# Kernel tuning notes

Hardware: AMD Instinct MI355X
Metric: run time of the kernel (lower is better)

## Reference

```python
import jax, jax.numpy as jnp
import numpy as np

B, N, D, H = 32, 512, 1024, 16
HD = D // H          # head_dim = 64
SEG = 64             # seg_num (router set size, softmax axis)
FACTOR = N           # einsum forces factor == seq_len


def setup_inputs() -> dict:
    key = jax.random.key(0)
    ks = jax.random.split(key, 12)
    s = 0.02
    return {
        "query": jax.random.normal(ks[0], (B, N, D), jnp.float32),
        "key":   jax.random.normal(ks[1], (B, N, D), jnp.float32),
        "value": jax.random.normal(ks[2], (B, N, D), jnp.float32),
        "router": jax.random.normal(ks[3], (SEG, FACTOR, HD), jnp.float32),
        "Wq": jax.random.normal(ks[4], (D, D), jnp.float32) * s,
        "bq": jnp.zeros((D,), jnp.float32),
        "Wk": jax.random.normal(ks[5], (D, D), jnp.float32) * s,
        "bk": jnp.zeros((D,), jnp.float32),
        "Wv": jax.random.normal(ks[6], (D, D), jnp.float32) * s,
        "bv": jnp.zeros((D,), jnp.float32),
        "Wo": jax.random.normal(ks[7], (D, D), jnp.float32) * s,
        "bo": jnp.zeros((D,), jnp.float32),
    }


def reference(query, key, value, router, Wq, bq, Wk, bk, Wv, bv, Wo, bo):
    b = query.shape[0]
    q = query @ Wq + bq                      # (B, N, D)
    k = key @ Wk + bk                        # computed but unused (faithful to source)
    v = value @ Wv + bv                      # computed but unused (faithful to source)
    # (B, N, H, HD) -> (B, H, N, HD)
    qh = q.reshape(b, -1, H, HD).transpose(0, 2, 1, 3)
    # torch: einsum('bnhd,bfhd->bnhf', q_bHnd, router_bSFd); shared 'h' = seq/factor
    # scores: (B, H, N, SEG); softmax over router/segment axis
    scores = jnp.einsum('bhnd,snd->bhns', qh, router)
    attn = jax.nn.softmax(scores, axis=-1)   # dropout = identity (eval mode)
    # combine: (B, H, N, HD)
    received = jnp.einsum('bhns,snd->bhnd', attn, router)
    received = received.transpose(0, 2, 1, 3).reshape(b, -1, D)
    output = received @ Wo + bo              # (B, N, D)
    return output, attn
```

## Files before the change

### kernel.cpp

```cpp
#include <hip/hip_runtime.h>

#define DEV __device__ __forceinline__

typedef __attribute__((ext_vector_type(8))) short bf16x8;
typedef __attribute__((ext_vector_type(4))) float f32x4;

constexpr int Bc  = 32;
constexpr int Nc  = 512;
constexpr int Dc  = 1024;
constexpr int Hc  = 16;
constexpr int HDc = 64;
constexpr int SEGc= 64;
constexpr int Mrows = Bc * Nc;

DEV unsigned short bf16r(float x) {
  union { float f; unsigned int u; } c; c.f = x;
  unsigned int r = (c.u + 0x7fffu + ((c.u >> 16) & 1u)) >> 16;
  return (unsigned short)r;
}

DEV void async_ld16(const void* g, void* l) {
  __builtin_amdgcn_global_load_lds(
      (const __attribute__((address_space(1))) void*)g,
      (__attribute__((address_space(3))) void*)l,
      16, 0, 0);
}

__global__ void cvt_bf16(const float* __restrict__ src,
                         unsigned short* __restrict__ dst, int n4) {
  int i = blockIdx.x * blockDim.x + threadIdx.x;
  if (i >= n4) return;
  float4 v = ((const float4*)src)[i];
  ushort4 o;
  o.x = bf16r(v.x); o.y = bf16r(v.y); o.z = bf16r(v.z); o.w = bf16r(v.w);
  ((ushort4*)dst)[i] = o;
}

__global__ void transpose_bf16(const float* __restrict__ src,
                               unsigned short* __restrict__ dst) {
  __shared__ float tile[32][33];
  int bx = blockIdx.x & 31, by = blockIdx.x >> 5;
  int tx = threadIdx.x & 31, ty = threadIdx.x >> 5;
  for (int i = 0; i < 4; ++i) {
    int r = ty + i * 8;
    tile[r][tx] = src[(size_t)(by * 32 + r) * 1024 + bx * 32 + tx];
  }
  __syncthreads();
  for (int i = 0; i < 4; ++i) {
    int r = ty + i * 8;
    dst[(size_t)(bx * 32 + r) * 1024 + by * 32 + tx] = bf16r(tile[tx][r]);
  }
}

template <bool OUT_F32>
__global__ __launch_bounds__(256)
void gemm_bt(const unsigned short* __restrict__ A,
             const unsigned short* __restrict__ BT,
             const float* __restrict__ bias,
             void* __restrict__ Cout) {
  constexpr int K = 1024, Nn = 1024, BM = 128, BN = 128, BK = 32;
  __shared__ unsigned short As[BM * BK];
  __shared__ unsigned short Bs[BN * BK];
  const int tid = threadIdx.x, lane = tid & 63, wave = tid >> 6;
  const int tm = blockIdx.x >> 3, tn = blockIdx.x & 7;
  const int wm = (wave >> 1) * 64, wn = (wave & 1) * 64;
  const int la = lane & 15, quad = lane >> 4, lb8 = quad * 8;

  f32x4 acc[4][4] = {};

  const int srow = tid >> 2;
  const int scol = (tid & 3) * 8;
  const unsigned short* Ag = A  + (size_t)(tm * BM + srow) * K + scol;
  const unsigned short* Bg = BT + (size_t)(tn * BN + srow) * K + scol;
  unsigned short* ldsA = As + wave * 512;
  unsigned short* ldsB = Bs + wave * 512;

  for (int k0 = 0; k0 < K; k0 += BK) {
    __syncthreads();
    async_ld16(Ag + k0,          ldsA);
    async_ld16(Ag + 64 * K + k0, ldsA + 2048);
    async_ld16(Bg + k0,          ldsB);
    async_ld16(Bg + 64 * K + k0, ldsB + 2048);
    __syncthreads();

    bf16x8 af[4], bfr[4];
#pragma unroll
    for (int i = 0; i < 4; ++i)
      af[i] = *(const bf16x8*)(As + (wm + i * 16 + la) * BK + lb8);
#pragma unroll
    for (int j = 0; j < 4; ++j)
      bfr[j] = *(const bf16x8*)(Bs + (wn + j * 16 + la) * BK + lb8);
#pragma unroll
    for (int i = 0; i < 4; ++i)
#pragma unroll
      for (int j = 0; j < 4; ++j)
        acc[i][j] = __builtin_amdgcn_mfma_f32_16x16x32_bf16(af[i], bfr[j],
                                                            acc[i][j], 0, 0, 0);
  }

  const int colbase = tn * BN + wn;
  float bv[4];
#pragma unroll
  for (int j = 0; j < 4; ++j) bv[j] = bias[colbase + j * 16 + la];

  float* eps = (wave < 2) ? ((float*)As) + wave * 1024
                          : ((float*)Bs) + (wave - 2) * 1024;
  const int rowbase = tm * BM + wm;

#pragma unroll
  for (int i = 0; i < 4; ++i) {
    __syncthreads();
#pragma unroll
    for (int j = 0; j < 4; ++j)
#pragma unroll
      for (int r = 0; r < 4; ++r)
        eps[(quad * 4 + r) * 64 + j * 16 + la] = acc[i][j][r] + bv[j];
    __syncthreads();
#pragma unroll
    for (int s = 0; s < 4; ++s) {
      int idx = s * 64 + lane;
      int row = idx >> 4, c4 = idx & 15;
      float4 v = *(const float4*)(eps + row * 64 + c4 * 4);
      size_t goff = (size_t)(rowbase + i * 16 + row) * Nn + colbase + c4 * 4;
      if (OUT_F32) {
        *(float4*)((float*)Cout + goff) = v;
      } else {
        ushort4 u;
        u.x = bf16r(v.x); u.y = bf16r(v.y); u.z = bf16r(v.z); u.w = bf16r(v.w);
        *(ushort4*)((unsigned short*)Cout + goff) = u;
      }
    }
  }
}

__global__ __launch_bounds__(256)
void router_mid(const unsigned short* __restrict__ qb,
                const unsigned short* __restrict__ routerb,
                float* __restrict__ attn_out,
                unsigned short* __restrict__ recv_out) {
  __shared__ unsigned short Rs [SEGc * HDc];
  __shared__ unsigned short RTs[HDc * SEGc];
  __shared__ unsigned short AT [4 * 16 * 64];
  __shared__ float          FW [4 * 16 * 64];

  const int n = blockIdx.x >> 1, half = blockIdx.x & 1;
  const int tid = threadIdx.x, lane = tid & 63, wave = tid >> 6;
  const int la = lane & 15, quad = lane >> 4, lb8 = quad * 8;

  {
    int c8 = (tid & 7) * 8;
    int s  = tid >> 3;
    async_ld16(routerb + ((size_t)s        * Nc + n) * HDc + c8, Rs + wave * 512);
    async_ld16(routerb + ((size_t)(s + 32) * Nc + n) * HDc + c8, Rs + 2048 + wave * 512);
  }
  __syncthreads();
  for (int i = 0; i < 16; ++i) {
    int idx = tid * 16 + i;
    RTs[(idx & 63) * 64 + (idx >> 6)] = Rs[idx];
  }
  __syncthreads();

  bf16x8 bs[4][2], br[4][2];
#pragma unroll
  for (int t = 0; t < 4; ++t)
#pragma unroll
    for (int kc = 0; kc < 2; ++kc) {
      bs[t][kc] = *(const bf16x8*)(Rs  + (t * 16 + la) * 64 + kc * 32 + lb8);
      br[t][kc] = *(const bf16x8*)(RTs + (t * 16 + la) * 64 + kc * 32 + lb8);
    }

  unsigned short* ATw = AT + wave * 1024;
  float*          FWw = FW + wave * 1024;

  for (int it = 0; it < 4; ++it) {
    const int bidx = half * 16 + wave * 4 + it;
    const unsigned short* qrow = qb + ((size_t)(bidx * Nc + n)) * Dc + la * 64;
    bf16x8 aq0 = *(const bf16x8*)(qrow + lb8);
    bf16x8 aq1 = *(const bf16x8*)(qrow + 32 + lb8);

    f32x4 sacc[4] = {};
#pragma unroll
    for (int t = 0; t < 4; ++t) {
      sacc[t] = __builtin_amdgcn_mfma_f32_16x16x32_bf16(aq0, bs[t][0], sacc[t], 0, 0, 0);
      sacc[t] = __builtin_amdgcn_mfma_f32_16x16x32_bf16(aq1, bs[t][1], sacc[t], 0, 0, 0);
    }

#pragma unroll
    for (int r = 0; r < 4; ++r) {
      float mx = fmaxf(fmaxf(sacc[0][r], sacc[1][r]), fmaxf(sacc[2][r], sacc[3][r]));
#pragma unroll
      for (int off = 1; off < 16; off <<= 1) mx = fmaxf(mx, __shfl_xor(mx, off));
      float e0 = __expf(sacc[0][r] - mx), e1 = __expf(sacc[1][r] - mx);
      float e2 = __expf(sacc[2][r] - mx), e3 = __expf(sacc[3][r] - mx);
      float sum = e0 + e1 + e2 + e3;
#pragma unroll
      for (int off = 1; off < 16; off <<= 1) sum += __shfl_xor(sum, off);
      float inv = 1.0f / sum;
      e0 *= inv; e1 *= inv; e2 *= inv; e3 *= inv;

      const int hrow = quad * 4 + r;
      float* fw = FWw + hrow * 64 + la;
      fw[0] = e0; fw[16] = e1; fw[32] = e2; fw[48] = e3;
      unsigned short* aw = ATw + hrow * 64 + la;
      aw[0] = bf16r(e0); aw[16] = bf16r(e1); aw[32] = bf16r(e2); aw[48] = bf16r(e3);
    }

    __asm__ volatile("s_waitcnt lgkmcnt(0)" ::: "memory");
    bf16x8 ar0 = *(const bf16x8*)(ATw + la * 64 + lb8);
    bf16x8 ar1 = *(const bf16x8*)(ATw + la * 64 + 32 + lb8);

    f32x4 racc[4] = {};
#pragma unroll
    for (int t = 0; t < 4; ++t) {
      racc[t] = __builtin_amdgcn_mfma_f32_16x16x32_bf16(ar0, br[t][0], racc[t], 0, 0, 0);
      racc[t] = __builtin_amdgcn_mfma_f32_16x16x32_bf16(ar1, br[t][1], racc[t], 0, 0, 0);
    }

#pragma unroll
    for (int s = 0; s < 4; ++s) {
      int idx = s * 64 + lane;
      int row = idx >> 4, c4 = idx & 15;
      float4 v = *(const float4*)(FWw + row * 64 + c4 * 4);
      *(float4*)(attn_out + ((size_t)(bidx * 16 + row) * Nc + n) * SEGc + c4 * 4) = v;
    }

#pragma unroll
    for (int r = 0; r < 4; ++r) {
      const int h = quad * 4 + r;
      unsigned short* aw = ATw + h * 64 + la;
#pragma unroll
      for (int t = 0; t < 4; ++t) aw[t * 16] = bf16r(racc[t][r]);
    }
    __asm__ volatile("s_waitcnt lgkmcnt(0)" ::: "memory");
    unsigned short* ro = recv_out + ((size_t)(bidx * Nc + n)) * Dc;
#pragma unroll
    for (int s = 0; s < 2; ++s)
      *(bf16x8*)(ro + s * 512 + lane * 8) = *(const bf16x8*)(ATw + s * 512 + lane * 8);
  }
}

extern "C" void kernel_launch(void* const* d_in, const int* in_sizes, int n_in,
                              void* d_out, int out_size, void* d_ws, size_t ws_size,
                              hipStream_t stream) {
  const float* query  = (const float*)d_in[0];
  const float* router = (const float*)d_in[3];
  const float* Wq     = (const float*)d_in[4];
  const float* bq     = (const float*)d_in[5];
  const float* Wo     = (const float*)d_in[10];
  const float* bo     = (const float*)d_in[11];

  float* out      = (float*)d_out;
  float* attn_out = out + (size_t)Bc * Nc * Dc;

  char* ws = (char*)d_ws;
  unsigned short* query_b  = (unsigned short*)(ws);
  unsigned short* q_b      = (unsigned short*)(ws + 33554432);
  unsigned short* recv_b   = (unsigned short*)(ws + 2u * 33554432);
  unsigned short* router_b = (unsigned short*)(ws + 3u * 33554432);
  unsigned short* WqT      = (unsigned short*)(ws + 3u * 33554432 + 4194304);
  unsigned short* WoT      = (unsigned short*)(ws + 3u * 33554432 + 4194304 + 2097152);

  cvt_bf16<<<16384, 256, 0, stream>>>(query,  query_b,  (Mrows * Dc) / 4);
  cvt_bf16<<<2048,  256, 0, stream>>>(router, router_b, (SEGc * Nc * HDc) / 4);
  transpose_bf16<<<1024, 256, 0, stream>>>(Wq, WqT);
  transpose_bf16<<<1024, 256, 0, stream>>>(Wo, WoT);

  gemm_bt<false><<<(Mrows / 128) * 8, 256, 0, stream>>>(query_b, WqT, bq, q_b);
  router_mid<<<2 * Nc, 256, 0, stream>>>(q_b, router_b, attn_out, recv_b);
  gemm_bt<true ><<<(Mrows / 128) * 8, 256, 0, stream>>>(recv_b, WoT, bo, out);
}
```

Before: 400.4 us.

## Fuse Q projection with router softmax mixing and pre-tile router weights

Replaces the separate query bf16 conversion, Q GEMM and router_mid kernels with one fused kernel. Each block computes the full 1024-wide Q projection for two sequence positions across all batches, converting query fp32 to bf16 on the fly with double-buffered LDS. It then runs the router score, softmax and combine steps straight from registers. This removes the round trips for the bf16 query copy and the q intermediate, but only 256 blocks of 512 threads are launched, which may underfill the GPU. It also uses a large LDS footprint and heavy accumulator register pressure.

```diff
diff --git a/kernel.cpp b/kernel.cpp
--- a/kernel.cpp
+++ b/kernel.cpp
@@ -24,16 +24,6 @@
       (const __attribute__((address_space(1))) void*)g,
       (__attribute__((address_space(3))) void*)l,
       16, 0, 0);
-}
-
-__global__ void cvt_bf16(const float* __restrict__ src,
-                         unsigned short* __restrict__ dst, int n4) {
-  int i = blockIdx.x * blockDim.x + threadIdx.x;
-  if (i >= n4) return;
-  float4 v = ((const float4*)src)[i];
-  ushort4 o;
-  o.x = bf16r(v.x); o.y = bf16r(v.y); o.z = bf16r(v.z); o.w = bf16r(v.w);
-  ((ushort4*)dst)[i] = o;
 }
 
 __global__ void transpose_bf16(const float* __restrict__ src,
@@ -52,15 +42,74 @@
   }
 }
 
+__global__ void wq_tile(const float* __restrict__ src,
+                        unsigned short* __restrict__ dst) {
+  __shared__ float tile[32][33];
+  int bx = blockIdx.x & 31, by = blockIdx.x >> 5;
+  int tx = threadIdx.x & 31, ty = threadIdx.x >> 5;
+  for (int i = 0; i < 4; ++i) {
+    int r = ty + i * 8;
+    tile[r][tx] = src[(size_t)(by * 32 + r) * 1024 + bx * 32 + tx];
+  }
+  __syncthreads();
+  if (ty < 4) {
+    int oct = ty;
+    unsigned short tmp[8];
+#pragma unroll
+    for (int e = 0; e < 8; ++e) tmp[e] = bf16r(tile[oct * 8 + e][tx]);
+    ushort4 u0, u1;
+    u0.x = tmp[0]; u0.y = tmp[1]; u0.z = tmp[2]; u0.w = tmp[3];
+    u1.x = tmp[4]; u1.y = tmp[5]; u1.z = tmp[6]; u1.w = tmp[7];
+    size_t idx = (size_t)by * 32768 + (size_t)oct * 8192 + (size_t)(bx * 32 + tx) * 8;
+    *(ushort4*)(dst + idx) = u0;
+    *(ushort4*)(dst + idx + 4) = u1;
+  }
+}
+
+__global__ void cvt_router2(const float* __restrict__ src,
+                            unsigned short* __restrict__ Rg,
+                            unsigned short* __restrict__ RTg) {
+  int nn = blockIdx.x;
+  int t  = threadIdx.x;
+  int s  = t >> 2, dq = (t & 3) * 16;
+  const float* p = src + ((size_t)s * 512 + nn) * 64 + dq;
+  float v[16];
+#pragma unroll
+  for (int i = 0; i < 16; i += 4) {
+    float4 f = *(const float4*)(p + i);
+    v[i] = f.x; v[i+1] = f.y; v[i+2] = f.z; v[i+3] = f.w;
+  }
+  unsigned short bv[16];
+#pragma unroll
+  for (int i = 0; i < 16; ++i) bv[i] = bf16r(v[i]);
+  unsigned short* rb = Rg + (size_t)nn * 4096 + s * 64;
+#pragma unroll
+  for (int o2 = 0; o2 < 2; ++o2) {
+    int oct  = (dq >> 3) + o2;
+    int phys = oct ^ (s & 7);
+    ushort4 a, b2;
+    a.x  = bv[o2*8+0]; a.y  = bv[o2*8+1]; a.z  = bv[o2*8+2]; a.w  = bv[o2*8+3];
+    b2.x = bv[o2*8+4]; b2.y = bv[o2*8+5]; b2.z = bv[o2*8+6]; b2.w = bv[o2*8+7];
+    *(ushort4*)(rb + phys * 8)     = a;
+    *(ushort4*)(rb + phys * 8 + 4) = b2;
+  }
+  unsigned short* tb = RTg + (size_t)nn * 4096;
+#pragma unroll
+  for (int i = 0; i < 16; ++i) {
+    int d = dq + i;
+    tb[d * 64 + (((s >> 3) ^ (d & 7)) * 8) + (s & 7)] = bv[i];
+  }
+}
+
 template <bool OUT_F32>
 __global__ __launch_bounds__(256)
 void gemm_bt(const unsigned short* __restrict__ A,
              const unsigned short* __restrict__ BT,
              const float* __restrict__ bias,
              void* __restrict__ Cout) {
-  constexpr int K = 1024, Nn = 1024, BM = 128, BN = 128, BK = 32;
+  constexpr int K = 1024, Nn = 1024, BM = 128, BK = 32;
   __shared__ unsigned short As[BM * BK];
-  __shared__ unsigned short Bs[BN * BK];
+  __shared__ unsigned short Bs[BM * BK];
   const int tid = threadIdx.x, lane = tid & 63, wave = tid >> 6;
   const int tm = blockIdx.x >> 3, tn = blockIdx.x & 7;
   const int wm = (wave >> 1) * 64, wn = (wave & 1) * 64;
@@ -71,7 +120,7 @@
   const int srow = tid >> 2;
   const int scol = (tid & 3) * 8;
   const unsigned short* Ag = A  + (size_t)(tm * BM + srow) * K + scol;
-  const unsigned short* Bg = BT + (size_t)(tn * BN + srow) * K + scol;
+  const unsigned short* Bg = BT + (size_t)(tn * BM + srow) * K + scol;
   unsigned short* ldsA = As + wave * 512;
   unsigned short* ldsB = Bs + wave * 512;
 
@@ -98,7 +147,7 @@
                                                             acc[i][j], 0, 0, 0);
   }
 
-  const int colbase = tn * BN + wn;
+  const int colbase = tn * BM + wn;
   float bv[4];
 #pragma unroll
   for (int j = 0; j < 4; ++j) bv[j] = bias[colbase + j * 16 + la];
@@ -133,109 +182,216 @@
   }
 }
 
-__global__ __launch_bounds__(256)
-void router_mid(const unsigned short* __restrict__ qb,
-                const unsigned short* __restrict__ routerb,
+__global__ __launch_bounds__(512, 2)
+void fused_qmid(const float* __restrict__ query,
+                const unsigned short* __restrict__ wqt,
+                const float* __restrict__ bq,
+                const unsigned short* __restrict__ Rg,
+                const unsigned short* __restrict__ RTg,
                 float* __restrict__ attn_out,
                 unsigned short* __restrict__ recv_out) {
-  __shared__ unsigned short Rs [SEGc * HDc];
-  __shared__ unsigned short RTs[HDc * SEGc];
-  __shared__ unsigned short AT [4 * 16 * 64];
-  __shared__ float          FW [4 * 16 * 64];
-
-  const int n = blockIdx.x >> 1, half = blockIdx.x & 1;
-  const int tid = threadIdx.x, lane = tid & 63, wave = tid >> 6;
-  const int la = lane & 15, quad = lane >> 4, lb8 = quad * 8;
+  __shared__ __align__(16) unsigned short lds[69632];
+  const int tid = threadIdx.x, lane = tid & 63, w = tid >> 6;
+  const int la = lane & 15, quad = lane >> 4;
+  const int n0 = blockIdx.x * 2;
+
+  f32x4 acc[4][8] = {};
+
+  const int arow = tid >> 3;
+  const int ag   = tid & 7;
+  const int a_b  = arow & 31, a_nl = arow >> 5;
+  const float* aq = query + ((size_t)(a_b * 512 + n0 + a_nl)) * 1024 + ag * 4;
+  const int a_lidx = (ag >> 1) * 512 + arow * 8 + (ag & 1) * 4;
+  const int bslot  = w * 512 + lane * 8;
 
   {
-    int c8 = (tid & 7) * 8;
-    int s  = tid >> 3;
-    async_ld16(routerb + ((size_t)s        * Nc + n) * HDc + c8, Rs + wave * 512);
-    async_ld16(routerb + ((size_t)(s + 32) * Nc + n) * HDc + c8, Rs + 2048 + wave * 512);
+    float4 qv = *(const float4*)(aq);
+#pragma unroll
+    for (int p = 0; p < 8; ++p)
+      async_ld16(wqt + p * 4096 + bslot, lds + p * 4096 + w * 512);
+    ushort4 u;
+    u.x = bf16r(qv.x); u.y = bf16r(qv.y); u.z = bf16r(qv.z); u.w = bf16r(qv.w);
+    *(ushort4*)(lds + 65536 + a_lidx) = u;
   }
   __syncthreads();
-  for (int i = 0; i < 16; ++i) {
-    int idx = tid * 16 + i;
-    RTs[(idx & 63) * 64 + (idx >> 6)] = Rs[idx];
+
+#pragma unroll 1
+  for (int kb = 0; kb < 32; ++kb) {
+    const int cur = kb & 1;
+    unsigned short* Bc_ = lds + cur * 32768;
+    unsigned short* Ac_ = lds + 65536 + cur * 2048;
+    unsigned short* Bn_ = lds + (cur ^ 1) * 32768;
+    unsigned short* An_ = lds + 65536 + (cur ^ 1) * 2048;
+
+    float4 qv;
+    if (kb < 31) {
+      qv = *(const float4*)(aq + (kb + 1) * 32);
+#pragma unroll
+      for (int p = 0; p < 8; ++p)
+        async_ld16(wqt + (size_t)(kb + 1) * 32768 + p * 4096 + bslot,
+                   Bn_ + p * 4096 + w * 512);
+    }
+
+    bf16x8 af[4], bfr[8];
+#pragma unroll
+    for (int rt = 0; rt < 4; ++rt)
+      af[rt] = *(const bf16x8*)(Ac_ + quad * 512 + (rt * 16 + la) * 8);
+#pragma unroll
+    for (int j = 0; j < 8; ++j)
+      bfr[j] = *(const bf16x8*)(Bc_ + quad * 8192 + ((w * 8 + j) * 16 + la) * 8);
+#pragma unroll
+    for (int rt = 0; rt < 4; ++rt)
+#pragma unroll
+      for (int j = 0; j < 8; ++j)
+        acc[rt][j] = __builtin_amdgcn_mfma_f32_16x16x32_bf16(af[rt], bfr[j],
+                                                             acc[rt][j], 0, 0, 0);
+    if (kb < 31) {
+      ushort4 u;
+      u.x = bf16r(qv.x); u.y = bf16r(qv.y); u.z = bf16r(qv.z); u.w = bf16r(qv.w);
+      *(ushort4*)(An_ + a_lidx) = u;
+    }
+    __syncthreads();
+  }
+
+  float bv[8];
+#pragma unroll
+  for (int j = 0; j < 8; ++j) bv[j] = bq[(w * 8 + j) * 16 + la];
+#pragma unroll
+  for (int rt = 0; rt < 4; ++rt)
+#pragma unroll
+    for (int j = 0; j < 8; ++j)
+#pragma unroll
+      for (int r = 0; r < 4; ++r) acc[rt][j][r] += bv[j];
+
+#pragma unroll
+  for (int q2 = 0; q2 < 4; ++q2) {
+    const unsigned short* srcb = (q2 < 2) ? (Rg  + (size_t)(n0 + q2)     * 4096)
+                                          : (RTg + (size_t)(n0 + q2 - 2) * 4096);
+    async_ld16(srcb + bslot, lds + 49152 + q2 * 4096 + w * 512);
   }
   __syncthreads();
 
-  bf16x8 bs[4][2], br[4][2];
-#pragma unroll
-  for (int t = 0; t < 4; ++t)
-#pragma unroll
-    for (int kc = 0; kc < 2; ++kc) {
-      bs[t][kc] = *(const bf16x8*)(Rs  + (t * 16 + la) * 64 + kc * 32 + lb8);
-      br[t][kc] = *(const bf16x8*)(RTs + (t * 16 + la) * 64 + kc * 32 + lb8);
+  unsigned short* Qs = lds + w * 6144;
+  unsigned short* AT = lds + w * 6144 + 3072;
+  const unsigned short* Rsb  = lds + 49152;
+  const unsigned short* RTsb = lds + 57344;
+
+#pragma unroll
+  for (int nl = 0; nl < 2; ++nl) {
+#pragma unroll
+    for (int hh = 0; hh < 2; ++hh) {
+      const int h  = w * 2 + hh;
+      const int nn = n0 + nl;
+
+#pragma unroll
+      for (int rt2 = 0; rt2 < 2; ++rt2)
+#pragma unroll
+        for (int j4 = 0; j4 < 4; ++j4)
+#pragma unroll
+          for (int r = 0; r < 4; ++r) {
+            int b_ = rt2 * 16 + quad * 4 + r;
+            int d_ = j4 * 16 + la;
+            Qs[b_ * 72 + d_] = bf16r(acc[nl * 2 + rt2][hh * 4 + j4][r]);
+          }
+
+      bf16x8 qf[2][2], rf[4][2];
+#pragma unroll
+      for (int bt = 0; bt < 2; ++bt)
+#pragma unroll
+        for (int kc = 0; kc < 2; ++kc)
+          qf[bt][kc] = *(const bf16x8*)(Qs + (bt * 16 + la) * 72 + (kc * 4 + quad) * 8);
+      const unsigned short* Rn = Rsb + nl * 4096;
+#pragma unroll
+      for (int st = 0; st < 4; ++st)
+#pragma unroll
+        for (int kc = 0; kc < 2; ++kc) {
+          int s_ = st * 16 + la;
+          rf[st][kc] = *(const bf16x8*)(Rn + s_ * 64 + ((kc * 4 + quad) ^ (s_ & 7)) * 8);
+        }
+
+      f32x4 sacc[2][4] = {};
+#pragma unroll
+      for (int bt = 0; bt < 2; ++bt)
+#pragma unroll
+        for (int st = 0; st < 4; ++st) {
+          sacc[bt][st] = __builtin_amdgcn_mfma_f32_16x16x32_bf16(rf[st][0], qf[bt][0], sacc[bt][st], 0, 0, 0);
+          sacc[bt][st] = __builtin_amdgcn_mfma_f32_16x16x32_bf16(rf[st][1], qf[bt][1], sacc[bt][st], 0, 0, 0);
+        }
+
+#pragma unroll
+      for (int bt = 0; bt < 2; ++bt) {
+        float mx = sacc[bt][0][0];
+#pragma unroll
+        for (int st = 0; st < 4; ++st)
+#pragma unroll
+          for (int r = 0; r < 4; ++r) mx = fmaxf(mx, sacc[bt][st][r]);
+        mx = fmaxf(mx, __shfl_xor(mx, 16));
+        mx = fmaxf(mx, __shfl_xor(mx, 32));
+        float sum = 0.f;
+#pragma unroll
+        for (int st = 0; st < 4; ++st)
+#pragma unroll
+          for (int r = 0; r < 4; ++r) {
+            float e = __expf(sacc[bt][st][r] - mx);
+            sacc[bt][st][r] = e; sum += e;
+          }
+        sum += __shfl_xor(sum, 16);
+        sum += __shfl_xor(sum, 32);
+        float inv = 1.0f / sum;
+#pragma unroll
+        for (int st = 0; st < 4; ++st) {
+          sacc[bt][st][0] *= inv; sacc[bt][st][1] *= inv;
+          sacc[bt][st][2] *= inv; sacc[bt][st][3] *= inv;
+        }
+        const int b_ = bt * 16 + la;
+        float* ao = attn_out + ((size_t)(b_ * 16 + h) * 512 + nn) * 64 + quad * 4;
+#pragma unroll
+        for (int st = 0; st < 4; ++st) {
+          *(float4*)(ao + st * 16) = *(float4*)(&sacc[bt][st]);
+          ushort4 u;
+          u.x = bf16r(sacc[bt][st][0]); u.y = bf16r(sacc[bt][st][1]);
+          u.z = bf16r(sacc[bt][st][2]); u.w = bf16r(sacc[bt][st][3]);
+          *(ushort4*)(AT + b_ * 72 + st * 16 + quad * 4) = u;
+        }
+      }
+
+      bf16x8 atf[2][2], rtf2[4][2];
+#pragma unroll
+      for (int bt = 0; bt < 2; ++bt)
+#pragma unroll
+        for (int kc = 0; kc < 2; ++kc)
+          atf[bt][kc] = *(const bf16x8*)(AT + (bt * 16 + la) * 72 + (kc * 4 + quad) * 8);
+      const unsigned short* RTn = RTsb + nl * 4096;
+#pragma unroll
+      for (int dt = 0; dt < 4; ++dt)
+#pragma unroll
+        for (int kc = 0; kc < 2; ++kc) {
+          int d_ = dt * 16 + la;
+          rtf2[dt][kc] = *(const bf16x8*)(RTn + d_ * 64 + ((kc * 4 + quad) ^ (d_ & 7)) * 8);
+        }
+      f32x4 racc[2][4] = {};
+#pragma unroll
+      for (int bt = 0; bt < 2; ++bt)
+#pragma unroll
+        for (int dt = 0; dt < 4; ++dt) {
+          racc[bt][dt] = __builtin_amdgcn_mfma_f32_16x16x32_bf16(rtf2[dt][0], atf[bt][0], racc[bt][dt], 0, 0, 0);
+          racc[bt][dt] = __builtin_amdgcn_mfma_f32_16x16x32_bf16(rtf2[dt][1], atf[bt][1], racc[bt][dt], 0, 0, 0);
+        }
+
+#pragma unroll
+      for (int bt = 0; bt < 2; ++bt) {
+        const int b_ = bt * 16 + la;
+        unsigned short* ro = recv_out + ((size_t)(b_ * 512 + nn)) * 1024
+                           + h * 64 + quad * 4;
+#pragma unroll
+        for (int dt = 0; dt < 4; ++dt) {
+          ushort4 u;
+          u.x = bf16r(racc[bt][dt][0]); u.y = bf16r(racc[bt][dt][1]);
+          u.z = bf16r(racc[bt][dt][2]); u.w = bf16r(racc[bt][dt][3]);
+          *(ushort4*)(ro + dt * 16) = u;
+        }
+      }
     }
-
-  unsigned short* ATw = AT + wave * 1024;
-  float*          FWw = FW + wave * 1024;
-
-  for (int it = 0; it < 4; ++it) {
-    const int bidx = half * 16 + wave * 4 + it;
-    const unsigned short* qrow = qb + ((size_t)(bidx * Nc + n)) * Dc + la * 64;
-    bf16x8 aq0 = *(const bf16x8*)(qrow + lb8);
-    bf16x8 aq1 = *(const bf16x8*)(qrow + 32 + lb8);
-
-    f32x4 sacc[4] = {};
-#pragma unroll
-    for (int t = 0; t < 4; ++t) {
-      sacc[t] = __builtin_amdgcn_mfma_f32_16x16x32_bf16(aq0, bs[t][0], sacc[t], 0, 0, 0);
-      sacc[t] = __builtin_amdgcn_mfma_f32_16x16x32_bf16(aq1, bs[t][1], sacc[t], 0, 0, 0);
-    }
-
-#pragma unroll
-    for (int r = 0; r < 4; ++r) {
-      float mx = fmaxf(fmaxf(sacc[0][r], sacc[1][r]), fmaxf(sacc[2][r], sacc[3][r]));
-#pragma unroll
-      for (int off = 1; off < 16; off <<= 1) mx = fmaxf(mx, __shfl_xor(mx, off));
-      float e0 = __expf(sacc[0][r] - mx), e1 = __expf(sacc[1][r] - mx);
-      float e2 = __expf(sacc[2][r] - mx), e3 = __expf(sacc[3][r] - mx);
-      float sum = e0 + e1 + e2 + e3;
-#pragma unroll
-      for (int off = 1; off < 16; off <<= 1) sum += __shfl_xor(sum, off);
-      float inv = 1.0f / sum;
-      e0 *= inv; e1 *= inv; e2 *= inv; e3 *= inv;
-
-      const int hrow = quad * 4 + r;
-      float* fw = FWw + hrow * 64 + la;
-      fw[0] = e0; fw[16] = e1; fw[32] = e2; fw[48] = e3;
-      unsigned short* aw = ATw + hrow * 64 + la;
-      aw[0] = bf16r(e0); aw[16] = bf16r(e1); aw[32] = bf16r(e2); aw[48] = bf16r(e3);
-    }
-
-    __asm__ volatile("s_waitcnt lgkmcnt(0)" ::: "memory");
-    bf16x8 ar0 = *(const bf16x8*)(ATw + la * 64 + lb8);
-    bf16x8 ar1 = *(const bf16x8*)(ATw + la * 64 + 32 + lb8);
-
-    f32x4 racc[4] = {};
-#pragma unroll
-    for (int t = 0; t < 4; ++t) {
-      racc[t] = __builtin_amdgcn_mfma_f32_16x16x32_bf16(ar0, br[t][0], racc[t], 0, 0, 0);
-      racc[t] = __builtin_amdgcn_mfma_f32_16x16x32_bf16(ar1, br[t][1], racc[t], 0, 0, 0);
-    }
-
-#pragma unroll
-    for (int s = 0; s < 4; ++s) {
-      int idx = s * 64 + lane;
-      int row = idx >> 4, c4 = idx & 15;
-      float4 v = *(const float4*)(FWw + row * 64 + c4 * 4);
-      *(float4*)(attn_out + ((size_t)(bidx * 16 + row) * Nc + n) * SEGc + c4 * 4) = v;
-    }
-
-#pragma unroll
-    for (int r = 0; r < 4; ++r) {
-      const int h = quad * 4 + r;
-      unsigned short* aw = ATw + h * 64 + la;
-#pragma unroll
-      for (int t = 0; t < 4; ++t) aw[t * 16] = bf16r(racc[t][r]);
-    }
-    __asm__ volatile("s_waitcnt lgkmcnt(0)" ::: "memory");
-    unsigned short* ro = recv_out + ((size_t)(bidx * Nc + n)) * Dc;
-#pragma unroll
-    for (int s = 0; s < 2; ++s)
-      *(bf16x8*)(ro + s * 512 + lane * 8) = *(const bf16x8*)(ATw + s * 512 + lane * 8);
   }
 }
 
@@ -253,19 +409,16 @@
   float* attn_out = out + (size_t)Bc * Nc * Dc;
 
   char* ws = (char*)d_ws;
-  unsigned short* query_b  = (unsigned short*)(ws);
-  unsigned short* q_b      = (unsigned short*)(ws + 33554432);
-  unsigned short* recv_b   = (unsigned short*)(ws + 2u * 33554432);
-  unsigned short* router_b = (unsigned short*)(ws + 3u * 33554432);
-  unsigned short* WqT      = (unsigned short*)(ws + 3u * 33554432 + 4194304);
-  unsigned short* WoT      = (unsigned short*)(ws + 3u * 33554432 + 4194304 + 2097152);
-
-  cvt_bf16<<<16384, 256, 0, stream>>>(query,  query_b,  (Mrows * Dc) / 4);
-  cvt_bf16<<<2048,  256, 0, stream>>>(router, router_b, (SEGc * Nc * HDc) / 4);
-  transpose_bf16<<<1024, 256, 0, stream>>>(Wq, WqT);
+  unsigned short* recv_b = (unsigned short*)(ws);
+  unsigned short* WqTile = (unsigned short*)(ws + 33554432u);
+  unsigned short* WoT    = (unsigned short*)(ws + 35651584u);
+  unsigned short* Rg     = (unsigned short*)(ws + 37748736u);
+  unsigned short* RTg    = (unsigned short*)(ws + 41943040u);
+
+  wq_tile       <<<1024, 256, 0, stream>>>(Wq, WqTile);
   transpose_bf16<<<1024, 256, 0, stream>>>(Wo, WoT);
-
-  gemm_bt<false><<<(Mrows / 128) * 8, 256, 0, stream>>>(query_b, WqT, bq, q_b);
-  router_mid<<<2 * Nc, 256, 0, stream>>>(q_b, router_b, attn_out, recv_b);
-  gemm_bt<true ><<<(Mrows / 128) * 8, 256, 0, stream>>>(recv_b, WoT, bo, out);
-}
+  cvt_router2   <<<512,  256, 0, stream>>>(router, Rg, RTg);
+  fused_qmid    <<<256,  512, 0, stream>>>(query, WqTile, bq, Rg, RTg,
+                                           attn_out, recv_b);
+  gemm_bt<true> <<<(Mrows / 128) * 8, 256, 0, stream>>>(recv_b, WoT, bo, out);
+}
```

Result: faster. 376.0 us (-6.1%).
